# Performance work log

Hardware: AMD Instinct MI355X
Metric: run time of the kernel (lower is better)

The kernel has to match this reference:

```python
import jax, jax.numpy as jnp
import numpy as np

B, S, DM, H = 8, 512, 1024, 16
D = DM // H            # head_dim = 64
NFEAT = 4              # len(feature_types)
N_DIST = 2 * 512 - 1   # max_utt_num*2-1 = 1023
N_DISC = 16 + 1        # len(DISCOURSE_RELATIONS)+1
N_COOC = 5 + 1


def setup_inputs() -> dict:
    key = jax.random.key(0)
    ks = jax.random.split(key, 24)
    inp = {}
    inp["query"] = jax.random.normal(ks[0], (B, S, DM), jnp.float32)
    inp["key"] = jax.random.normal(ks[1], (B, S, DM), jnp.float32)
    inp["value"] = jax.random.normal(ks[2], (B, S, DM), jnp.float32)
    inp["distance_adj"] = jax.random.randint(ks[3], (B, S, S), 0, N_DIST).astype(jnp.int32)
    inp["speaker_adj"] = jax.random.uniform(ks[4], (B, S, S), jnp.float32)
    inp["discourse_adj"] = jax.random.randint(ks[5], (B, S, S), 0, N_DISC).astype(jnp.int32)
    inp["cooccurrence_adj"] = jax.random.randint(ks[6], (B, S, S), 0, N_COOC).astype(jnp.int32)
    inp["mask"] = jnp.ones((B, 1, 1, S), jnp.int32)
    w = lambda k, shape: jax.random.normal(k, shape, jnp.float32) * 0.02
    inp["Wq"] = w(ks[7], (DM, DM)); inp["bq"] = jnp.zeros((DM,), jnp.float32)
    inp["Wk"] = w(ks[8], (DM, DM)); inp["bk"] = jnp.zeros((DM,), jnp.float32)
    inp["Wv"] = w(ks[9], (DM, DM)); inp["bv"] = jnp.zeros((DM,), jnp.float32)
    inp["Wo"] = w(ks[10], (DM, DM)); inp["bo"] = jnp.zeros((DM,), jnp.float32)
    inp["dist_embed"] = w(ks[11], (N_DIST, 1))
    inp["disc_embed"] = w(ks[12], (N_DISC, 1)).at[0].set(0.0)  # padding_idx=0
    inp["cooc_embed"] = w(ks[13], (N_COOC, 1)).at[0].set(0.0)  # padding_idx=0
    inp["fcw"] = w(ks[14], (H, NFEAT))       # per-head 1x1 conv weights
    inp["fcb"] = jnp.zeros((H,), jnp.float32)
    inp["cw"] = w(ks[15], (2,))              # combine conv weights
    inp["cb"] = jnp.zeros((), jnp.float32)
    return inp


def reference(query, key, value, distance_adj, speaker_adj, discourse_adj,
              cooccurrence_adj, mask, Wq, bq, Wk, bk, Wv, bv, Wo, bo,
              dist_embed, disc_embed, cooc_embed, fcw, fcb, cw, cb):
    scale = jnp.asarray(D ** 0.5, query.dtype)
    # Linear projections, split heads -> [B, H, S, D]
    split = lambda x: x.reshape(B, S, H, D).transpose(0, 2, 1, 3)
    Q = split(query @ Wq.T + bq)
    K = split(key @ Wk.T + bk)
    V = split(value @ Wv.T + bv)
    energy = jnp.einsum('bhqd,bhkd->bhqk', Q, K) / scale  # [B,H,S,S]
    # Adjacency feature maps in feature_types order: distance, speaker, discourse, cooccurrence
    dist = dist_embed[distance_adj, 0]
    disc = disc_embed[discourse_adj, 0] * (discourse_adj != 0)
    cooc = cooc_embed[cooccurrence_adj, 0] * (cooccurrence_adj != 0)
    feature_map = jnp.stack([dist, speaker_adj, disc, cooc], axis=1)  # [B,4,S,S]
    # Per-head 1x1 conv over the 4 feature channels + relu
    feat = jax.nn.relu(jnp.einsum('hc,bcij->bhij', fcw, feature_map)
                       + fcb[None, :, None, None])       # [B,H,S,S]
    # Combine conv (1x1, 2 channels -> 1) + relu
    energy = jax.nn.relu(cw[0] * energy + cw[1] * feat + cb)
    energy = jnp.where(mask == 0, -jnp.inf, energy)
    attention = jax.nn.softmax(energy, axis=-1)           # [B,H,S,S]
    x = jnp.einsum('bhqk,bhkd->bhqd', attention, V)       # dropout p=0 (eval)
    x = x.transpose(0, 2, 1, 3).reshape(B, S, DM)
    x = x @ Wo.T + bo
    return x, attention
```

## Files before the change

kernel.cpp:

```cpp
#include <hip/hip_runtime.h>

using short8 = __attribute__((ext_vector_type(8))) short;
using f32x4  = __attribute__((ext_vector_type(4))) float;

__device__ __forceinline__ unsigned short f2bf(float x) {
    union { float f; unsigned u; } v; v.f = x;
    unsigned u = v.u;
    unsigned r = (u + 0x7fffu + ((u >> 16) & 1u)) >> 16;
    return (unsigned short)r;
}
__device__ __forceinline__ float bf2f(unsigned short h) {
    union { unsigned u; float f; } v; v.u = ((unsigned)h) << 16;
    return v.f;
}

__device__ __forceinline__ void async16(const void* g, void* l) {
    __builtin_amdgcn_global_load_lds(
        (const __attribute__((address_space(1))) void*)g,
        (__attribute__((address_space(3))) void*)l, 16, 0, 0);
}

__global__ __launch_bounds__(256) void cvt_qkv(
    const float* __restrict__ q, const float* __restrict__ k, const float* __restrict__ v,
    unsigned short* __restrict__ dst)
{
    int z = blockIdx.z;
    const float* src = (z == 0) ? q : ((z == 1) ? k : v);
    unsigned short* o = dst + (size_t)z * 4194304;
    size_t i = ((size_t)blockIdx.x * 256 + threadIdx.x) * 8;
    float4 a = *(const float4*)(src + i);
    float4 b = *(const float4*)(src + i + 4);
    ushort4 lo, hi;
    lo.x = f2bf(a.x); lo.y = f2bf(a.y); lo.z = f2bf(a.z); lo.w = f2bf(a.w);
    hi.x = f2bf(b.x); hi.y = f2bf(b.y); hi.z = f2bf(b.z); hi.w = f2bf(b.w);
    *(ushort4*)(o + i) = lo;
    *(ushort4*)(o + i + 4) = hi;
}

__global__ __launch_bounds__(256) void cvt_w(
    const float* __restrict__ wq, const float* __restrict__ wk,
    const float* __restrict__ wv, const float* __restrict__ wo,
    unsigned short* __restrict__ dst)
{
    int z = blockIdx.z;
    const float* src = (z == 0) ? wq : ((z == 1) ? wk : ((z == 2) ? wv : wo));
    unsigned short* o = dst + (size_t)z * 1048576;
    size_t i = ((size_t)blockIdx.x * 256 + threadIdx.x) * 8;
    float4 a = *(const float4*)(src + i);
    float4 b = *(const float4*)(src + i + 4);
    ushort4 lo, hi;
    lo.x = f2bf(a.x); lo.y = f2bf(a.y); lo.z = f2bf(a.z); lo.w = f2bf(a.w);
    hi.x = f2bf(b.x); hi.y = f2bf(b.y); hi.z = f2bf(b.z); hi.w = f2bf(b.w);
    *(ushort4*)(o + i) = lo;
    *(ushort4*)(o + i + 4) = hi;
}

__global__ __launch_bounds__(256) void feat_kernel(
    const int* __restrict__ dist_adj, const float* __restrict__ spk,
    const int* __restrict__ disc_adj, const int* __restrict__ cooc_adj,
    const float* __restrict__ dist_emb, const float* __restrict__ disc_emb,
    const float* __restrict__ cooc_emb, const float* __restrict__ fcw,
    const float* __restrict__ fcb, const float* __restrict__ cw,
    unsigned short* __restrict__ G)
{
    __shared__ float s_dist[1023];
    __shared__ float s_disc[17];
    __shared__ float s_cooc[6];
    __shared__ float s_fcw[64];
    __shared__ float s_fcb[16];
    int tid = threadIdx.x;
    for (int i = tid; i < 1023; i += 256) s_dist[i] = dist_emb[i];
    if (tid < 17) s_disc[tid] = disc_emb[tid];
    if (tid < 6)  s_cooc[tid] = cooc_emb[tid];
    if (tid < 64) s_fcw[tid]  = fcw[tid];
    if (tid < 16) s_fcb[tid]  = fcb[tid];
    __syncthreads();
    float cw1 = cw[1];

    int bx = blockIdx.x;
    int k  = (bx & 1) * 256 + tid;
    int qq = (bx >> 1) & 127;
    int b  = bx >> 8;

    size_t abase = ((size_t)b * 512 + qq * 4) * 512 + k;
    float f0[4], f1[4], f2[4], f3[4];
#pragma unroll
    for (int r = 0; r < 4; ++r) {
        size_t a = abase + (size_t)r * 512;
        int dd = dist_adj[a];
        f1[r]  = spk[a];
        int dc = disc_adj[a];
        int cc = cooc_adj[a];
        f0[r] = s_dist[dd];
        f2[r] = dc ? s_disc[dc] : 0.f;
        f3[r] = cc ? s_cooc[cc] : 0.f;
    }

    size_t gq = ((size_t)b * 16 * 128 + qq) * 512 + k;
#pragma unroll
    for (int h = 0; h < 16; ++h) {
        float w0 = s_fcw[h*4+0], w1 = s_fcw[h*4+1], w2 = s_fcw[h*4+2], w3 = s_fcw[h*4+3];
        float bb = s_fcb[h];
        ushort4 o;
        o.x = f2bf(fmaxf(w0*f0[0] + w1*f1[0] + w2*f2[0] + w3*f3[0] + bb, 0.f) * cw1);
        o.y = f2bf(fmaxf(w0*f0[1] + w1*f1[1] + w2*f2[1] + w3*f3[1] + bb, 0.f) * cw1);
        o.z = f2bf(fmaxf(w0*f0[2] + w1*f1[2] + w2*f2[2] + w3*f3[2] + bb, 0.f) * cw1);
        o.w = f2bf(fmaxf(w0*f0[3] + w1*f1[3] + w2*f2[3] + w3*f3[3] + bb, 0.f) * cw1);
        *(ushort4*)(G + (gq + (size_t)h * 65536) * 4) = o;
    }
}

template<int OMODE>
__device__ __forceinline__ void gemm_bf16_body(
    const unsigned short* __restrict__ A, const unsigned short* __restrict__ W,
    const float* __restrict__ bias, void* __restrict__ outp, int m0, int n0)
{
    __shared__ __align__(16) unsigned short As[128 * 32];
    __shared__ __align__(16) unsigned short Bs[128 * 32];
    int tid = threadIdx.x;
    int lane = tid & 63, wid = tid >> 6;
    int wx = wid & 1, wy = wid >> 1;
    int lanelo = lane & 15, hi8 = (lane >> 4) * 8;
    int rowc = lane >> 2;
    int colc = (lane & 3) * 8;

    f32x4 acc[4][4];
#pragma unroll
    for (int i = 0; i < 4; ++i)
#pragma unroll
        for (int j = 0; j < 4; ++j) {
            acc[i][j][0] = 0.f; acc[i][j][1] = 0.f; acc[i][j][2] = 0.f; acc[i][j][3] = 0.f;
        }

    for (int kk = 0; kk < 32; ++kk) {
        int k0 = kk * 32;
        __syncthreads();
#pragma unroll
        for (int p = 0; p < 2; ++p) {
            int c = 2 * wid + p;
            int row = c * 16 + rowc;
            async16(A + (size_t)(m0 + row) * 1024 + k0 + colc, As + c * 512);
        }
#pragma unroll
        for (int p = 0; p < 2; ++p) {
            int c = 2 * wid + p;
            int row = c * 16 + rowc;
            async16(W + (size_t)(n0 + row) * 1024 + k0 + colc, Bs + c * 512);
        }
        __syncthreads();

        short8 af[4], bfr[4];
#pragma unroll
        for (int i = 0; i < 4; ++i)
            af[i] = *(const short8*)(As + (wy*64 + i*16 + lanelo) * 32 + hi8);
#pragma unroll
        for (int j = 0; j < 4; ++j)
            bfr[j] = *(const short8*)(Bs + (wx*64 + j*16 + lanelo) * 32 + hi8);
#pragma unroll
        for (int i = 0; i < 4; ++i)
#pragma unroll
            for (int j = 0; j < 4; ++j)
                acc[i][j] = __builtin_amdgcn_mfma_f32_16x16x32_bf16(af[i], bfr[j], acc[i][j], 0, 0, 0);
    }

    float bia[4];
#pragma unroll
    for (int j = 0; j < 4; ++j) bia[j] = bias[n0 + wx*64 + j*16 + lanelo];
#pragma unroll
    for (int i = 0; i < 4; ++i) {
        int mbase = m0 + wy*64 + i*16 + (lane >> 4) * 4;
#pragma unroll
        for (int j = 0; j < 4; ++j) {
            int n = n0 + wx*64 + j*16 + lanelo;
#pragma unroll
            for (int r = 0; r < 4; ++r) {
                int m = mbase + r;
                float val = acc[i][j][r] + bia[j];
                if (OMODE == 0) {
                    unsigned short* o = (unsigned short*)outp;
                    o[((size_t)((m >> 9) * 16 + (n >> 6)) * 512 + (m & 511)) * 64 + (n & 63)] = f2bf(val);
                } else {
                    float* o = (float*)outp;
                    o[(size_t)m * 1024 + n] = val;
                }
            }
        }
    }
}

__global__ __launch_bounds__(256) void gemm_qkv(
    const unsigned short* __restrict__ Abf, const unsigned short* __restrict__ Wbf,
    const float* __restrict__ bq, const float* __restrict__ bk, const float* __restrict__ bv,
    unsigned short* Qb, unsigned short* Kb, unsigned short* Vb)
{
    int z = blockIdx.z;
    const unsigned short* A = Abf + (size_t)z * 4194304;
    const unsigned short* W = Wbf + (size_t)z * 1048576;
    const float* bias = (z == 0) ? bq : ((z == 1) ? bk : bv);
    unsigned short* o = (z == 0) ? Qb : ((z == 1) ? Kb : Vb);
    gemm_bf16_body<0>(A, W, bias, o, blockIdx.x * 128, blockIdx.y * 128);
}

__global__ __launch_bounds__(256) void gemm_proj(
    const unsigned short* __restrict__ xh, const unsigned short* __restrict__ Wo,
    const float* __restrict__ bo, float* __restrict__ out)
{
    gemm_bf16_body<1>(xh, Wo, bo, out, blockIdx.x * 128, blockIdx.y * 128);
}

__global__ __launch_bounds__(256) void transpose_v(const unsigned short* __restrict__ Vb,
                                                   unsigned short* __restrict__ Vt)
{
    __shared__ __align__(16) unsigned short T[64][72];
    int tid = threadIdx.x;
    int s0 = blockIdx.x * 64;
    int bh = blockIdx.z * 16 + blockIdx.y;
#pragma unroll
    for (int p = 0; p < 2; ++p) {
        int c = p * 256 + tid;
        int row = c >> 3, kc = (c & 7) * 8;
        uint4 v = *(const uint4*)(Vb + ((size_t)bh * 512 + s0 + row) * 64 + kc);
        *(uint4*)&T[row][kc] = v;
    }
    __syncthreads();
#pragma unroll
    for (int p = 0; p < 2; ++p) {
        int c = p * 256 + tid;
        int d = c >> 3, sc = (c & 7) * 8;
        unsigned vv[4];
#pragma unroll
        for (int i = 0; i < 4; ++i) {
            unsigned lo = T[sc + 2*i][d];
            unsigned hi = T[sc + 2*i + 1][d];
            vv[i] = lo | (hi << 16);
        }
        uint4 o; o.x = vv[0]; o.y = vv[1]; o.z = vv[2]; o.w = vv[3];
        *(uint4*)(Vt + ((size_t)bh * 64 + d) * 512 + s0 + sc) = o;
    }
}

__global__ __launch_bounds__(256, 2) void attn_kernel(
    const unsigned short* __restrict__ Qb, const unsigned short* __restrict__ Kb,
    const unsigned short* __restrict__ Vt, const unsigned short* __restrict__ G,
    const int* __restrict__ mask, const float* __restrict__ cw,
    const float* __restrict__ cb, float* __restrict__ attn_out,
    unsigned short* __restrict__ xh)
{
    __shared__ __align__(16) unsigned short Qs[64][72];
    __shared__ __align__(16) unsigned short Ks[128][72];
    __shared__ __align__(16) unsigned short Vs[64][40];
    __shared__ __align__(16) unsigned short Ps[4][16][40];
    __shared__ __align__(16) float PT[4][16][68];
    __shared__ int s_mask[512];

    int tid = threadIdx.x;
    int lane = tid & 63, w = tid >> 6;
    int lanelo = lane & 15, hi8 = (lane >> 4) * 8;
    int hi2 = lane >> 4;
    int qt = blockIdx.x, h = blockIdx.y, b = blockIdx.z;
    int bh = b * 16 + h;
    float qs  = cw[0] * 0.125f;
    float cbv = cb[0];

    s_mask[tid]       = mask[b * 512 + tid];
    s_mask[tid + 256] = mask[b * 512 + tid + 256];
#pragma unroll
    for (int p = 0; p < 2; ++p) {
        int c = p * 256 + tid;
        int row = c >> 3, kc = (c & 7) * 8;
        uint4 v = *(const uint4*)(Qb + ((size_t)bh * 512 + qt * 64 + row) * 64 + kc);
        *(uint4*)&Qs[row][kc] = v;
    }
    __syncthreads();

    short8 aq[2];
    aq[0] = *(const short8*)&Qs[w * 16 + lanelo][hi8];
    aq[1] = *(const short8*)&Qs[w * 16 + lanelo][32 + hi8];
    int qrow = qt * 64 + w * 16 + hi2 * 4;
    int qq   = qt * 16 + w * 4 + hi2;
    const unsigned short* gbase = G + ((size_t)bh * 128 + qq) * 2048;

    float P[32][4];
#pragma unroll 1
    for (int kt = 0; kt < 4; ++kt) {
        ushort4 g[8];
#pragma unroll
        for (int j = 0; j < 8; ++j)
            g[j] = *(const ushort4*)(gbase + (kt * 8 + j) * 64 + lanelo * 4);
        __syncthreads();
#pragma unroll
        for (int p = 0; p < 4; ++p) {
            int c = p * 256 + tid;
            int row = c >> 3, kc = (c & 7) * 8;
            uint4 v = *(const uint4*)(Kb + ((size_t)bh * 512 + kt * 128 + row) * 64 + kc);
            *(uint4*)&Ks[row][kc] = v;
        }
        __syncthreads();
#pragma unroll
        for (int j = 0; j < 8; ++j) {
            short8 b0 = *(const short8*)&Ks[j * 16 + lanelo][hi8];
            short8 b1 = *(const short8*)&Ks[j * 16 + lanelo][32 + hi8];
            f32x4 acc; acc[0] = 0.f; acc[1] = 0.f; acc[2] = 0.f; acc[3] = 0.f;
            acc = __builtin_amdgcn_mfma_f32_16x16x32_bf16(aq[0], b0, acc, 0, 0, 0);
            acc = __builtin_amdgcn_mfma_f32_16x16x32_bf16(aq[1], b1, acc, 0, 0, 0);
            int jj = kt * 8 + j;
            int kcol = jj * 16 + lanelo;
            int mk = s_mask[kcol];
            float gf[4] = { bf2f(g[j].x), bf2f(g[j].y), bf2f(g[j].z), bf2f(g[j].w) };
#pragma unroll
            for (int r = 0; r < 4; ++r) {
                float e = qs * acc[r] + gf[r] + cbv;
                e = fmaxf(e, 0.f);
                P[jj][r] = mk ? __expf(e) : 0.f;
            }
        }
    }

    float inv[4];
#pragma unroll
    for (int r = 0; r < 4; ++r) {
        float s = 0.f;
#pragma unroll
        for (int jj = 0; jj < 32; ++jj) s += P[jj][r];
        s += __shfl_xor(s, 1, 64);
        s += __shfl_xor(s, 2, 64);
        s += __shfl_xor(s, 4, 64);
        s += __shfl_xor(s, 8, 64);
        inv[r] = 1.0f / s;
    }

    {
        float* PTw = &PT[w][0][0];
        float* op  = attn_out + ((size_t)bh * 512 + qt * 64 + w * 16) * 512;
#pragma unroll
        for (int c = 0; c < 8; ++c) {
#pragma unroll
            for (int jc = 0; jc < 4; ++jc) {
                int jj = c * 4 + jc;
#pragma unroll
                for (int r = 0; r < 4; ++r)
                    PTw[(hi2 * 4 + r) * 68 + jc * 16 + lanelo] = P[jj][r] * inv[r];
            }
            asm volatile("s_waitcnt lgkmcnt(0)" ::: "memory");
#pragma unroll
            for (int p = 0; p < 4; ++p) {
                int row = p * 4 + hi2;
                float4 v4 = *(const float4*)&PTw[row * 68 + lanelo * 4];
                *(float4*)(op + (size_t)row * 512 + c * 64 + lanelo * 4) = v4;
            }
            asm volatile("" ::: "memory");
        }
    }

    f32x4 xacc[4];
#pragma unroll
    for (int jf = 0; jf < 4; ++jf) { xacc[jf][0]=0.f; xacc[jf][1]=0.f; xacc[jf][2]=0.f; xacc[jf][3]=0.f; }
#pragma unroll 1
    for (int ks = 0; ks < 16; ++ks) {
        __syncthreads();
        {
            int d = tid >> 2, kc = (tid & 3) * 8;
            uint4 v = *(const uint4*)(Vt + ((size_t)bh * 64 + d) * 512 + ks * 32 + kc);
            *(uint4*)&Vs[d][kc] = v;
        }
#pragma unroll
        for (int ff = 0; ff < 2; ++ff) {
            int f = ks * 2 + ff;
#pragma unroll
            for (int r = 0; r < 4; ++r)
                Ps[w][hi2 * 4 + r][ff * 16 + lanelo] = f2bf(P[f][r]);
        }
        __syncthreads();
        short8 ap8 = *(const short8*)&Ps[w][lanelo][hi8];
#pragma unroll
        for (int jf = 0; jf < 4; ++jf) {
            short8 bv = *(const short8*)&Vs[jf * 16 + lanelo][hi8];
            xacc[jf] = __builtin_amdgcn_mfma_f32_16x16x32_bf16(ap8, bv, xacc[jf], 0, 0, 0);
        }
    }

    {
        unsigned short* XT = (unsigned short*)&PT[w][0][0];
        asm volatile("" ::: "memory");
#pragma unroll
        for (int jf = 0; jf < 4; ++jf)
#pragma unroll
            for (int r = 0; r < 4; ++r)
                XT[(hi2 * 4 + r) * 68 + jf * 16 + lanelo] = f2bf(xacc[jf][r] * inv[r]);
        asm volatile("s_waitcnt lgkmcnt(0)" ::: "memory");
        unsigned short* xp = xh + ((size_t)b * 512 + qt * 64 + w * 16) * 1024 + h * 64;
#pragma unroll
        for (int p = 0; p < 4; ++p) {
            int row = p * 4 + hi2;
            ushort4 v = *(const ushort4*)&XT[row * 68 + lanelo * 4];
            *(ushort4*)(xp + (size_t)row * 1024 + lanelo * 4) = v;
        }
    }
}

extern "C" void kernel_launch(void* const* d_in, const int* in_sizes, int n_in,
                              void* d_out, int out_size, void* d_ws, size_t ws_size,
                              hipStream_t stream) {
    (void)in_sizes; (void)n_in; (void)out_size; (void)ws_size;
    const float* query    = (const float*)d_in[0];
    const float* key      = (const float*)d_in[1];
    const float* value    = (const float*)d_in[2];
    const int*   dist_adj = (const int*)d_in[3];
    const float* spk      = (const float*)d_in[4];
    const int*   disc_adj = (const int*)d_in[5];
    const int*   cooc_adj = (const int*)d_in[6];
    const int*   maskp    = (const int*)d_in[7];
    const float* Wq = (const float*)d_in[8];  const float* bq = (const float*)d_in[9];
    const float* Wk = (const float*)d_in[10]; const float* bk = (const float*)d_in[11];
    const float* Wv = (const float*)d_in[12]; const float* bv = (const float*)d_in[13];
    const float* Wo = (const float*)d_in[14]; const float* bo = (const float*)d_in[15];
    const float* dist_emb = (const float*)d_in[16];
    const float* disc_emb = (const float*)d_in[17];
    const float* cooc_emb = (const float*)d_in[18];
    const float* fcw = (const float*)d_in[19];
    const float* fcb = (const float*)d_in[20];
    const float* cw  = (const float*)d_in[21];
    const float* cbp = (const float*)d_in[22];

    char* w = (char*)d_ws;
    unsigned short* Qb  = (unsigned short*)(w);
    unsigned short* Kb  = (unsigned short*)(w + 8388608);
    unsigned short* Vb  = (unsigned short*)(w + 16777216);
    unsigned short* Vt  = (unsigned short*)(w + 25165824);
    unsigned short* xh  = (unsigned short*)(w + 33554432);
    unsigned short* G   = (unsigned short*)(w + 41943040);
    unsigned short* Abf = G;
    unsigned short* Wbf = (unsigned short*)(w + 109051904);

    float* out_x    = (float*)d_out;
    float* attn_out = ((float*)d_out) + 4194304;

    cvt_qkv<<<dim3(2048, 1, 3), 256, 0, stream>>>(query, key, value, Abf);
    cvt_w<<<dim3(512, 1, 4), 256, 0, stream>>>(Wq, Wk, Wv, Wo, Wbf);
    gemm_qkv<<<dim3(32, 8, 3), 256, 0, stream>>>(Abf, Wbf, bq, bk, bv, Qb, Kb, Vb);
    transpose_v<<<dim3(8, 16, 8), 256, 0, stream>>>(Vb, Vt);
    feat_kernel<<<2048, 256, 0, stream>>>(dist_adj, spk, disc_adj, cooc_adj,
                                          dist_emb, disc_emb, cooc_emb, fcw, fcb, cw, G);
    attn_kernel<<<dim3(8, 16, 8), 256, 0, stream>>>(Qb, Kb, Vt, G, maskp, cw, cbp,
                                                    attn_out, xh);
    gemm_proj<<<dim3(32, 8), 256, 0, stream>>>(xh, Wbf + 3145728, bo, out_x);
}
```

Measured before the change: 462.1 us.

## Alias attention LDS buffers, raise occupancy, and remap blocks XCD-locally

```diff
diff --git a/kernel.cpp b/kernel.cpp
--- a/kernel.cpp
+++ b/kernel.cpp
@@ -239,26 +239,33 @@
     }
 }
 
-__global__ __launch_bounds__(256, 2) void attn_kernel(
+__global__ __launch_bounds__(256, 4) void attn_kernel(
     const unsigned short* __restrict__ Qb, const unsigned short* __restrict__ Kb,
     const unsigned short* __restrict__ Vt, const unsigned short* __restrict__ G,
     const int* __restrict__ mask, const float* __restrict__ cw,
     const float* __restrict__ cb, float* __restrict__ attn_out,
     unsigned short* __restrict__ xh)
 {
-    __shared__ __align__(16) unsigned short Qs[64][72];
-    __shared__ __align__(16) unsigned short Ks[128][72];
-    __shared__ __align__(16) unsigned short Vs[64][40];
-    __shared__ __align__(16) unsigned short Ps[4][16][40];
-    __shared__ __align__(16) float PT[4][16][68];
-    __shared__ int s_mask[512];
+    __shared__ __align__(16) char smem[39936];
+    unsigned short (*Qs)[72]     = (unsigned short (*)[72])smem;
+    unsigned short (*Ks)[72]     = (unsigned short (*)[72])(smem + 9216);
+    float          (*PT)[16][68] = (float (*)[16][68])smem;
+    unsigned short (*Vs)[40]     = (unsigned short (*)[40])(smem + 27648);
+    unsigned short (*Ps)[16][40] = (unsigned short (*)[16][40])(smem + 32768);
+    int* s_mask = (int*)(smem + 37888);
 
     int tid = threadIdx.x;
     int lane = tid & 63, w = tid >> 6;
     int lanelo = lane & 15, hi8 = (lane >> 4) * 8;
     int hi2 = lane >> 4;
-    int qt = blockIdx.x, h = blockIdx.y, b = blockIdx.z;
-    int bh = b * 16 + h;
+
+    int lin = blockIdx.x;
+    int xcd = lin & 7;
+    int s   = lin >> 3;
+    int bh  = xcd * 16 + (s >> 3);
+    int qt  = s & 7;
+    int b   = bh >> 4, h = bh & 15;
+
     float qs  = cw[0] * 0.125f;
     float cbv = cb[0];
 
@@ -315,18 +322,19 @@
             }
         }
     }
+    __syncthreads();
 
     float inv[4];
 #pragma unroll
     for (int r = 0; r < 4; ++r) {
-        float s = 0.f;
-#pragma unroll
-        for (int jj = 0; jj < 32; ++jj) s += P[jj][r];
-        s += __shfl_xor(s, 1, 64);
-        s += __shfl_xor(s, 2, 64);
-        s += __shfl_xor(s, 4, 64);
-        s += __shfl_xor(s, 8, 64);
-        inv[r] = 1.0f / s;
+        float s0 = 0.f;
+#pragma unroll
+        for (int jj = 0; jj < 32; ++jj) s0 += P[jj][r];
+        s0 += __shfl_xor(s0, 1, 64);
+        s0 += __shfl_xor(s0, 2, 64);
+        s0 += __shfl_xor(s0, 4, 64);
+        s0 += __shfl_xor(s0, 8, 64);
+        inv[r] = 1.0f / s0;
     }
 
     {
@@ -380,7 +388,7 @@
     }
 
     {
-        unsigned short* XT = (unsigned short*)&PT[w][0][0];
+        unsigned short* XT = (unsigned short*)(PT + w);
         asm volatile("" ::: "memory");
 #pragma unroll
         for (int jf = 0; jf < 4; ++jf)
@@ -441,7 +449,7 @@
     transpose_v<<<dim3(8, 16, 8), 256, 0, stream>>>(Vb, Vt);
     feat_kernel<<<2048, 256, 0, stream>>>(dist_adj, spk, disc_adj, cooc_adj,
                                           dist_emb, disc_emb, cooc_emb, fcw, fcb, cw, G);
-    attn_kernel<<<dim3(8, 16, 8), 256, 0, stream>>>(Qb, Kb, Vt, G, maskp, cw, cbp,
-                                                    attn_out, xh);
+    attn_kernel<<<dim3(1024, 1, 1), 256, 0, stream>>>(Qb, Kb, Vt, G, maskp, cw, cbp,
+                                                      attn_out, xh);
     gemm_proj<<<dim3(32, 8), 256, 0, stream>>>(xh, Wbf + 3145728, bo, out_x);
 }
```

New measurement: 468.0 us. Within noise of the previous version (+1.3%).
